# Kernel tuning notes

Measured on AMD Instinct MI355X. Metric: run time of the kernel, lower is better.

## Reference

```python
import jax, jax.numpy as jnp
import numpy as np
import math

B, T, N_EMBD, HEAD_SIZE = 8, 2048, 768, 128


def setup_inputs() -> dict:
    key = jax.random.key(0)
    ks = jax.random.split(key, 7)
    s = 0.02
    return {
        "x": jax.random.normal(ks[0], (B, T, N_EMBD), dtype=jnp.float32),
        "Wq": jax.random.normal(ks[1], (N_EMBD, HEAD_SIZE), dtype=jnp.float32) * s,
        "bq": jax.random.normal(ks[2], (HEAD_SIZE,), dtype=jnp.float32) * s,
        "Wk": jax.random.normal(ks[3], (N_EMBD, HEAD_SIZE), dtype=jnp.float32) * s,
        "bk": jax.random.normal(ks[4], (HEAD_SIZE,), dtype=jnp.float32) * s,
        "Wv": jax.random.normal(ks[5], (N_EMBD, HEAD_SIZE), dtype=jnp.float32) * s,
        "bv": jax.random.normal(ks[6], (HEAD_SIZE,), dtype=jnp.float32) * s,
    }


def reference(x, Wq, bq, Wk, bk, Wv, bv):
    # x: [B, T, n_embd]
    Tlen = x.shape[1]
    q = x @ Wq + bq  # [B, T, hs]
    k = x @ Wk + bk
    v = x @ Wv + bv
    scores = jnp.einsum('bqd,bkd->bqk', q, k)  # [B, T, T]
    causal = jnp.tril(jnp.ones((Tlen, Tlen), dtype=bool))
    # original masks with -inf first, then divides by sqrt(head_size); -inf/scale == -inf,
    # so mask-then-scale is mathematically identical.
    scores = jnp.where(causal, scores, -jnp.inf) / math.sqrt(q.shape[-1])
    weights = jax.nn.softmax(scores, axis=-1)
    # dropout p=0.0 (inference/reference) -> identity
    out = jnp.einsum('bqk,bkd->bqd', weights, v)  # [B, T, hs]
    return out
```

## Files before the change

kernel.cpp:

```cpp
#include <hip/hip_runtime.h>

#define B_ 8
#define T_ 2048
#define E_ 768
#define D_ 128
#define SCALE2 (0.08838834764831845f * 1.4426950408889634f)
#define MFIX 8.0f

typedef _Float16 h8 __attribute__((ext_vector_type(8)));
typedef _Float16 h4 __attribute__((ext_vector_type(4)));
typedef _Float16 h2 __attribute__((ext_vector_type(2)));
typedef float f4 __attribute__((ext_vector_type(4)));

typedef __attribute__((address_space(1))) unsigned int as1_u32;
typedef __attribute__((address_space(3))) unsigned int as3_u32;

__device__ __forceinline__ void gl_lds16(const void* g, void* l) {
    __builtin_amdgcn_global_load_lds((const as1_u32*)g, (as3_u32*)l, 16, 0, 0);
}

__global__ __launch_bounds__(256) void w_prep(
    const float* __restrict__ Wq, const float* __restrict__ Wk,
    const float* __restrict__ Wv, _Float16* __restrict__ Wh)
{
    __shared__ float tile[64][129];
    const int y = blockIdx.x / 12, kc = blockIdx.x % 12;
    const float* W = (y == 0) ? Wq : (y == 1) ? Wk : Wv;
    const int k0 = kc * 64, t = threadIdx.x;
#pragma unroll
    for (int i = 0; i < 32; ++i) {
        const int idx = i * 256 + t;
        tile[idx >> 7][idx & 127] = W[(size_t)(k0 + (idx >> 7)) * D_ + (idx & 127)];
    }
    __syncthreads();
    const int n = t >> 1, hf = t & 1;
#pragma unroll
    for (int j = 0; j < 4; ++j) {
        const int kk = hf * 32 + j * 8;
        h8 hv;
#pragma unroll
        for (int e = 0; e < 8; ++e) hv[e] = (_Float16)tile[kk + e][n];
        *(h8*)&Wh[(size_t)(y * 128 + n) * E_ + k0 + kk] = hv;
    }
}

__global__ __launch_bounds__(512, 1) void qkv_fused(
    const float* __restrict__ x, const _Float16* __restrict__ Wh,
    const float* __restrict__ bq, const float* __restrict__ bk,
    const float* __restrict__ bv,
    _Float16* __restrict__ Qh, _Float16* __restrict__ Kh,
    _Float16* __restrict__ Vt)
{
    __shared__ _Float16 As[2][64 * 64];
    __shared__ _Float16 Bs[2][384 * 64];

    const int t = threadIdx.x;
    const int lane = t & 63, w = t >> 6;
    const int quad = lane >> 4, col = lane & 15;
    const int m0 = blockIdx.x * 64;

    f4 acc[4][3];
#pragma unroll
    for (int mt = 0; mt < 4; ++mt)
#pragma unroll
        for (int nt = 0; nt < 3; ++nt) acc[mt][nt] = (f4){0.f, 0.f, 0.f, 0.f};

    const int brl = lane >> 3, bc = lane & 7;
    const int xr_ = t >> 3, xcb = (t & 7) * 8;

    float4 xv[2];

#define LOAD_X(kb)                                                          \
    {   const float* xr = &x[(size_t)(m0 + xr_) * E_ + (kb) + xcb];         \
        xv[0] = *(const float4*)(xr);                                       \
        xv[1] = *(const float4*)(xr + 4);                                   }

#define STAGE_B(dst, kb)                                                    \
    _Pragma("unroll")                                                       \
    for (int i = 0; i < 6; ++i) {                                           \
        const int R = w * 48 + i * 8;                                       \
        const int r = R + brl;                                              \
        gl_lds16(Wh + (size_t)r * E_ + (kb) + 8 * (bc ^ (r & 7)), &(dst)[R * 64]); }

#define WRITE_A(dst)                                                        \
    _Pragma("unroll")                                                       \
    for (int i = 0; i < 2; ++i) {                                           \
        h4 hv; hv[0] = (_Float16)xv[i].x; hv[1] = (_Float16)xv[i].y;        \
        hv[2] = (_Float16)xv[i].z; hv[3] = (_Float16)xv[i].w;               \
        const int kk4 = xcb + 4 * i;                                        \
        *(h4*)&(dst)[xr_ * 64 + (((kk4 >> 3) ^ (xr_ & 7)) << 3) + (kk4 & 7)] = hv; }

    LOAD_X(0);
    STAGE_B(Bs[0], 0);
    asm volatile("s_waitcnt vmcnt(6)" ::: "memory");
    WRITE_A(As[0]);
    asm volatile("s_waitcnt vmcnt(0) lgkmcnt(0)" ::: "memory");
    __builtin_amdgcn_s_barrier();

#pragma unroll 2
    for (int it = 0; it < 12; ++it) {
        const int c = it & 1;
        if (it < 11) {
            LOAD_X((it + 1) * 64);
            STAGE_B(Bs[c ^ 1], (it + 1) * 64);
        }
#pragma unroll
        for (int ks = 0; ks < 2; ++ks) {
            const int sc = ((ks << 2) + quad) ^ (col & 7);
            h8 a[4], bf[3];
#pragma unroll
            for (int mt = 0; mt < 4; ++mt)
                a[mt] = *(const h8*)&As[c][(mt * 16 + col) * 64 + (sc << 3)];
#pragma unroll
            for (int nt = 0; nt < 3; ++nt)
                bf[nt] = *(const h8*)&Bs[c][(w * 48 + nt * 16 + col) * 64 + (sc << 3)];
#pragma unroll
            for (int mt = 0; mt < 4; ++mt)
#pragma unroll
                for (int nt = 0; nt < 3; ++nt)
                    acc[mt][nt] = __builtin_amdgcn_mfma_f32_16x16x32_f16(
                        a[mt], bf[nt], acc[mt][nt], 0, 0, 0);
        }
        if (it < 11) {
            asm volatile("s_waitcnt vmcnt(6)" ::: "memory");
            WRITE_A(As[c ^ 1]);
            asm volatile("s_waitcnt vmcnt(0) lgkmcnt(0)" ::: "memory");
            __builtin_amdgcn_s_barrier();
        }
    }

    const float* bp[3] = {bq, bk, bv};
    _Float16* Cs = &Bs[0][0];
#pragma unroll
    for (int nt = 0; nt < 3; ++nt) {
        const int n16 = w * 48 + nt * 16;
        const int y = n16 >> 7, nl = n16 & 127;
        const float bb = bp[y][nl + col];
#pragma unroll
        for (int mt = 0; mt < 4; ++mt)
#pragma unroll
            for (int reg = 0; reg < 4; ++reg) {
                const int m = mt * 16 + quad * 4 + reg;
                Cs[m * 384 + n16 + col] = (_Float16)(acc[mt][nt][reg] + bb);
            }
    }
    __syncthreads();

    {
        const int m = t >> 3, seg = t & 7;
#pragma unroll
        for (int j = 0; j < 4; ++j) {
            const int n = seg * 8 + j * 64;
            const h8 v = *(const h8*)&Cs[m * 384 + n];
            if (n < 128) *(h8*)&Qh[(size_t)(m0 + m) * D_ + n] = v;
            else         *(h8*)&Kh[(size_t)(m0 + m) * D_ + (n - 128)] = v;
        }
    }
    {
        const int vn = t & 127, part = t >> 7;
        const int bidx = m0 >> 11, tt0 = m0 & 2047;
#pragma unroll
        for (int j = 0; j < 2; ++j) {
            const int ms = part * 16 + j * 8;
            h8 hv;
#pragma unroll
            for (int e = 0; e < 8; ++e) hv[e] = Cs[(ms + e) * 384 + 256 + vn];
            *(h8*)&Vt[((size_t)bidx * D_ + vn) * T_ + tt0 + ms] = hv;
        }
    }
#undef LOAD_X
#undef STAGE_B
#undef WRITE_A
}

__global__ __launch_bounds__(256, 2) void flash_attn(
    const _Float16* __restrict__ Qh,
    const _Float16* __restrict__ Kh,
    const _Float16* __restrict__ Vt,
    float* __restrict__ out)
{
    __shared__ __align__(16) char smem[70656];
    _Float16* Ks = (_Float16*)smem;
    _Float16* Vs = (_Float16*)(smem + 32768);
    _Float16* Pb = (_Float16*)(smem + 65536);

    const int t = threadIdx.x, lane = t & 63, w = t >> 6;
    const int quad = lane >> 4, col = lane & 15;
    const int id = blockIdx.x;
    const int b = id & 7;
    const int k6 = id >> 3;
    const int j32 = (k6 < 32) ? (63 - k6) : (k6 - 32);
    const int qw = w & 1, kh = w >> 1;
    const int qbase = j32 * 32;
    const int qrow0 = qbase + qw * 16;
    const int nk = (j32 >> 1) + 1;

    h8 qf[4];
    const _Float16* Qp = Qh + ((size_t)b * T_ + qrow0 + col) * D_ + quad * 8;
#pragma unroll
    for (int ks = 0; ks < 4; ++ks) qf[ks] = *(const h8*)(Qp + ks * 32);
    asm volatile("s_waitcnt vmcnt(0)" ::: "memory");

    f4 o[8];
#pragma unroll
    for (int i = 0; i < 8; ++i) o[i] = (f4){0.f, 0.f, 0.f, 0.f};
    float l_st = 0.f;

    const _Float16* Kb = Kh + (size_t)b * T_ * D_;
    const _Float16* Vb = Vt + (size_t)b * D_ * T_;
    const int krl = lane >> 4, kc = lane & 15;
    const int vrl = lane >> 3, vc = lane & 7;
    const int cx = col & 7;

    auto stage = [&](int buf, int kbase) __attribute__((always_inline)) {
        _Float16* KsB = Ks + buf * 8192;
        _Float16* VsB = Vs + buf * 8192;
#pragma unroll
        for (int i = 0; i < 4; ++i) {
            const int R = w * 16 + i * 4;
            const int r = R + krl;
            gl_lds16(Kb + (size_t)(kbase + r) * D_ + 8 * (kc ^ (r & 7)), KsB + R * D_);
        }
#pragma unroll
        for (int i = 0; i < 4; ++i) {
            const int R = w * 32 + i * 8;
            const int d = R + vrl;
            gl_lds16(Vb + (size_t)d * T_ + kbase + 8 * (vc ^ (d & 7)), VsB + R * 64);
        }
    };

    _Float16* Pw = Pb + w * 640;

    auto step = [&](int ti, int buf, bool mask) __attribute__((always_inline)) {
        const _Float16* KsB = Ks + buf * 8192;
        const _Float16* VsB = Vs + buf * 8192;

        f4 s[2];
        s[0] = (f4){0.f, 0.f, 0.f, 0.f};
        s[1] = (f4){0.f, 0.f, 0.f, 0.f};
        __builtin_amdgcn_s_setprio(1);
#pragma unroll
        for (int nt = 0; nt < 2; ++nt) {
            const int r = kh * 32 + nt * 16 + col;
#pragma unroll
            for (int ks = 0; ks < 4; ++ks) {
                const h8 kf = *(const h8*)(KsB + r * D_ + 8 * (((ks << 2) + quad) ^ cx));
                s[nt] = __builtin_amdgcn_mfma_f32_16x16x32_f16(kf, qf[ks], s[nt], 0, 0, 0);
            }
        }
        __builtin_amdgcn_s_setprio(0);

        const int qr = qrow0 + col;
        if (mask) {
#pragma unroll
            for (int nt = 0; nt < 2; ++nt) {
                const int key = ti * 64 + kh * 32 + nt * 16 + quad * 4;
#pragma unroll
                for (int reg = 0; reg < 4; ++reg) {
                    const float sv = s[nt][reg] * SCALE2 - MFIX;
                    s[nt][reg] = (key + reg <= qr) ? sv : -1e30f;
                }
            }
        } else {
#pragma unroll
            for (int nt = 0; nt < 2; ++nt)
#pragma unroll
                for (int reg = 0; reg < 4; ++reg)
                    s[nt][reg] = s[nt][reg] * SCALE2 - MFIX;
        }
#pragma unroll
        for (int nt = 0; nt < 2; ++nt)
#pragma unroll
            for (int reg = 0; reg < 4; ++reg) {
                const float p = __builtin_amdgcn_exp2f(s[nt][reg]);
                s[nt][reg] = p;
                l_st += p;
            }

#pragma unroll
        for (int nt = 0; nt < 2; ++nt) {
            h2 p0; p0[0] = (_Float16)s[nt][0]; p0[1] = (_Float16)s[nt][1];
            h2 p1; p1[0] = (_Float16)s[nt][2]; p1[1] = (_Float16)s[nt][3];
            *(h2*)&Pw[col * 40 + nt * 16 + quad * 4]     = p0;
            *(h2*)&Pw[col * 40 + nt * 16 + quad * 4 + 2] = p1;
        }
        const h8 pa = *(const h8*)&Pw[col * 40 + quad * 8];

        __builtin_amdgcn_s_setprio(1);
#pragma unroll
        for (int n2 = 0; n2 < 8; ++n2) {
            const int d = n2 * 16 + col;
            const h8 vf = *(const h8*)(VsB + d * 64 + 8 * ((kh * 4 + quad) ^ (d & 7)));
            o[n2] = __builtin_amdgcn_mfma_f32_16x16x32_f16(vf, pa, o[n2], 0, 0, 0);
        }
        __builtin_amdgcn_s_setprio(0);
    };

    stage(0, 0);
    const bool evenJ = ((j32 & 1) == 0);
    for (int ti = 0; ti < nk; ++ti) {
        const int cur = ti & 1;
        if (ti + 1 < nk) {
            stage(cur ^ 1, (ti + 1) << 6);
            asm volatile("s_waitcnt vmcnt(8)" ::: "memory");
        } else {
            asm volatile("s_waitcnt vmcnt(0)" ::: "memory");
        }
        __builtin_amdgcn_s_barrier();
        const bool last = (ti == nk - 1);
        if (!(last && evenJ && kh == 1)) {
            const bool mask = last && (kh == (j32 & 1));
            step(ti, cur, mask);
        }
        __builtin_amdgcn_s_barrier();
    }

    l_st += __shfl_xor(l_st, 16);
    l_st += __shfl_xor(l_st, 32);

    float* Os = (float*)smem;
    float* Lx = (float*)(smem + 16896);
    const int qloc = qw * 16 + col;

    __syncthreads();
    if (kh == 1) {
        if (quad == 0) Lx[qloc] = l_st;
#pragma unroll
        for (int n2 = 0; n2 < 8; ++n2)
#pragma unroll
            for (int reg = 0; reg < 4; ++reg)
                Os[qloc * 132 + n2 * 16 + quad * 4 + reg] = o[n2][reg];
    }
    __syncthreads();
    if (kh == 0) {
        const float inv = 1.0f / (l_st + Lx[qloc]);
#pragma unroll
        for (int n2 = 0; n2 < 8; ++n2)
#pragma unroll
            for (int reg = 0; reg < 4; ++reg) {
                const int d = n2 * 16 + quad * 4 + reg;
                Os[qloc * 132 + d] = (o[n2][reg] + Os[qloc * 132 + d]) * inv;
            }
    }
    __syncthreads();
    {
        const int row = t >> 3, d0 = (t & 7) * 16;
        float* op = &out[((size_t)b * T_ + qbase + row) * D_ + d0];
#pragma unroll
        for (int j = 0; j < 4; ++j)
            *(float4*)(op + j * 4) = *(const float4*)&Os[row * 132 + d0 + j * 4];
    }
}

extern "C" void kernel_launch(void* const* d_in, const int* in_sizes, int n_in,
                              void* d_out, int out_size, void* d_ws, size_t ws_size,
                              hipStream_t stream) {
    const float* x  = (const float*)d_in[0];
    const float* Wq = (const float*)d_in[1];
    const float* bq = (const float*)d_in[2];
    const float* Wk = (const float*)d_in[3];
    const float* bk = (const float*)d_in[4];
    const float* Wv = (const float*)d_in[5];
    const float* bv = (const float*)d_in[6];

    _Float16* Qh = (_Float16*)d_ws;
    _Float16* Kh = Qh + (size_t)B_ * T_ * D_;
    _Float16* Vt = Kh + (size_t)B_ * T_ * D_;
    _Float16* Wh = (_Float16*)d_out;

    w_prep<<<dim3(36), dim3(256), 0, stream>>>(Wq, Wk, Wv, Wh);
    qkv_fused<<<dim3(B_ * T_ / 64), dim3(512), 0, stream>>>(
        x, Wh, bq, bk, bv, Qh, Kh, Vt);
    flash_attn<<<dim3(512), dim3(256), 0, stream>>>(Qh, Kh, Vt, (float*)d_out);
}
```

Baseline: 142.4 us.

## Prefetch x two stages ahead in QKV GEMM; use bpermute for P in attention

The QKV projection GEMM now double-buffers the fp32 x register loads and issues them two K-steps ahead, with adjusted vmcnt waits, so global latency for x is hidden behind more MFMA work. In flash attention, the P-matrix register transpose through LDS (store then reload) is replaced by cross-lane ds_bpermute shuffles and selects. This removes the P scratch buffer, trimming LDS to 64KB, which may help occupancy. The trade-off is more registers for the extra x buffer and eight bpermutes per step in place of LDS writes plus one read.

```diff
diff --git a/kernel.cpp b/kernel.cpp
--- a/kernel.cpp
+++ b/kernel.cpp
@@ -11,12 +11,18 @@
 typedef _Float16 h4 __attribute__((ext_vector_type(4)));
 typedef _Float16 h2 __attribute__((ext_vector_type(2)));
 typedef float f4 __attribute__((ext_vector_type(4)));
+typedef unsigned int u4 __attribute__((ext_vector_type(4)));
 
 typedef __attribute__((address_space(1))) unsigned int as1_u32;
 typedef __attribute__((address_space(3))) unsigned int as3_u32;
 
 __device__ __forceinline__ void gl_lds16(const void* g, void* l) {
     __builtin_amdgcn_global_load_lds((const as1_u32*)g, (as3_u32*)l, 16, 0, 0);
+}
+
+__device__ __forceinline__ unsigned int pkh2(float a, float b) {
+    h2 t; t[0] = (_Float16)a; t[1] = (_Float16)b;
+    return __builtin_bit_cast(unsigned int, t);
 }
 
 __global__ __launch_bounds__(256) void w_prep(
@@ -68,12 +74,12 @@
     const int brl = lane >> 3, bc = lane & 7;
     const int xr_ = t >> 3, xcb = (t & 7) * 8;
 
-    float4 xv[2];
-
-#define LOAD_X(kb)                                                          \
+    float4 xv2[2][2];
+
+#define LOAD_X(dst, kb)                                                     \
     {   const float* xr = &x[(size_t)(m0 + xr_) * E_ + (kb) + xcb];         \
-        xv[0] = *(const float4*)(xr);                                       \
-        xv[1] = *(const float4*)(xr + 4);                                   }
+        (dst)[0] = *(const float4*)(xr);                                    \
+        (dst)[1] = *(const float4*)(xr + 4);                                }
 
 #define STAGE_B(dst, kb)                                                    \
     _Pragma("unroll")                                                       \
@@ -82,28 +88,27 @@
         const int r = R + brl;                                              \
         gl_lds16(Wh + (size_t)r * E_ + (kb) + 8 * (bc ^ (r & 7)), &(dst)[R * 64]); }
 
-#define WRITE_A(dst)                                                        \
+#define WRITE_A(dst, src)                                                   \
     _Pragma("unroll")                                                       \
     for (int i = 0; i < 2; ++i) {                                           \
-        h4 hv; hv[0] = (_Float16)xv[i].x; hv[1] = (_Float16)xv[i].y;        \
-        hv[2] = (_Float16)xv[i].z; hv[3] = (_Float16)xv[i].w;               \
+        h4 hv; hv[0] = (_Float16)(src)[i].x; hv[1] = (_Float16)(src)[i].y;  \
+        hv[2] = (_Float16)(src)[i].z; hv[3] = (_Float16)(src)[i].w;         \
         const int kk4 = xcb + 4 * i;                                        \
         *(h4*)&(dst)[xr_ * 64 + (((kk4 >> 3) ^ (xr_ & 7)) << 3) + (kk4 & 7)] = hv; }
 
-    LOAD_X(0);
+    LOAD_X(xv2[0], 0);
     STAGE_B(Bs[0], 0);
-    asm volatile("s_waitcnt vmcnt(6)" ::: "memory");
-    WRITE_A(As[0]);
-    asm volatile("s_waitcnt vmcnt(0) lgkmcnt(0)" ::: "memory");
+    LOAD_X(xv2[1], 64);
+    asm volatile("s_waitcnt vmcnt(8)" ::: "memory");
+    WRITE_A(As[0], xv2[0]);
+    asm volatile("s_waitcnt vmcnt(2) lgkmcnt(0)" ::: "memory");
     __builtin_amdgcn_s_barrier();
 
 #pragma unroll 2
     for (int it = 0; it < 12; ++it) {
         const int c = it & 1;
-        if (it < 11) {
-            LOAD_X((it + 1) * 64);
-            STAGE_B(Bs[c ^ 1], (it + 1) * 64);
-        }
+        if (it < 11) STAGE_B(Bs[c ^ 1], (it + 1) * 64);
+        if (it < 10) LOAD_X(xv2[c], (it + 2) * 64);
 #pragma unroll
         for (int ks = 0; ks < 2; ++ks) {
             const int sc = ((ks << 2) + quad) ^ (col & 7);
@@ -122,9 +127,11 @@
                         a[mt], bf[nt], acc[mt][nt], 0, 0, 0);
         }
         if (it < 11) {
-            asm volatile("s_waitcnt vmcnt(6)" ::: "memory");
-            WRITE_A(As[c ^ 1]);
-            asm volatile("s_waitcnt vmcnt(0) lgkmcnt(0)" ::: "memory");
+            if (it < 10) { asm volatile("s_waitcnt vmcnt(8)" ::: "memory"); }
+            else         { asm volatile("s_waitcnt vmcnt(6)" ::: "memory"); }
+            WRITE_A(As[c ^ 1], xv2[c ^ 1]);
+            if (it < 10) { asm volatile("s_waitcnt vmcnt(2) lgkmcnt(0)" ::: "memory"); }
+            else         { asm volatile("s_waitcnt vmcnt(0) lgkmcnt(0)" ::: "memory"); }
             __builtin_amdgcn_s_barrier();
         }
     }
@@ -179,10 +186,9 @@
     const _Float16* __restrict__ Vt,
     float* __restrict__ out)
 {
-    __shared__ __align__(16) char smem[70656];
+    __shared__ __align__(16) char smem[65536];
     _Float16* Ks = (_Float16*)smem;
     _Float16* Vs = (_Float16*)(smem + 32768);
-    _Float16* Pb = (_Float16*)(smem + 65536);
 
     const int t = threadIdx.x, lane = t & 63, w = t >> 6;
     const int quad = lane >> 4, col = lane & 15;
@@ -211,6 +217,9 @@
     const int krl = lane >> 4, kc = lane & 15;
     const int vrl = lane >> 3, vc = lane & 7;
     const int cx = col & 7;
+    const int addr0 = ((((quad & 1) << 1) + 0) * 16 + col) << 2;
+    const int addr1 = ((((quad & 1) << 1) + 1) * 16 + col) << 2;
+    const int ntd = quad >> 1;
 
     auto stage = [&](int buf, int kbase) __attribute__((always_inline)) {
         _Float16* KsB = Ks + buf * 8192;
@@ -229,8 +238,6 @@
         }
     };
 
-    _Float16* Pw = Pb + w * 640;
-
     auto step = [&](int ti, int buf, bool mask) __attribute__((always_inline)) {
         const _Float16* KsB = Ks + buf * 8192;
         const _Float16* VsB = Vs + buf * 8192;
@@ -277,14 +284,24 @@
                 l_st += p;
             }
 
-#pragma unroll
-        for (int nt = 0; nt < 2; ++nt) {
-            h2 p0; p0[0] = (_Float16)s[nt][0]; p0[1] = (_Float16)s[nt][1];
-            h2 p1; p1[0] = (_Float16)s[nt][2]; p1[1] = (_Float16)s[nt][3];
-            *(h2*)&Pw[col * 40 + nt * 16 + quad * 4]     = p0;
-            *(h2*)&Pw[col * 40 + nt * 16 + quad * 4 + 2] = p1;
-        }
-        const h8 pa = *(const h8*)&Pw[col * 40 + quad * 8];
+        const unsigned int w00 = pkh2(s[0][0], s[0][1]);
+        const unsigned int w01 = pkh2(s[0][2], s[0][3]);
+        const unsigned int w10 = pkh2(s[1][0], s[1][1]);
+        const unsigned int w11 = pkh2(s[1][2], s[1][3]);
+        const unsigned int a00 = __builtin_amdgcn_ds_bpermute(addr0, w00);
+        const unsigned int a10 = __builtin_amdgcn_ds_bpermute(addr0, w10);
+        const unsigned int a01 = __builtin_amdgcn_ds_bpermute(addr0, w01);
+        const unsigned int a11 = __builtin_amdgcn_ds_bpermute(addr0, w11);
+        const unsigned int b00 = __builtin_amdgcn_ds_bpermute(addr1, w00);
+        const unsigned int b10 = __builtin_amdgcn_ds_bpermute(addr1, w10);
+        const unsigned int b01 = __builtin_amdgcn_ds_bpermute(addr1, w01);
+        const unsigned int b11 = __builtin_amdgcn_ds_bpermute(addr1, w11);
+        u4 pu;
+        pu[0] = ntd ? a10 : a00;
+        pu[1] = ntd ? a11 : a01;
+        pu[2] = ntd ? b10 : b00;
+        pu[3] = ntd ? b11 : b01;
+        const h8 pa = __builtin_bit_cast(h8, pu);
 
         __builtin_amdgcn_s_setprio(1);
 #pragma unroll
```

Result: no change. 144.5 us (+1.4%).
